# Kernel optimization log

Measured on AMD Instinct MI355X. Metric: run time of the kernel, lower is better.

Reference implementation:

```python
import jax, jax.numpy as jnp
import numpy as np
from math import tan, atan

N = 4_000_000
W_PX, H_PX = 1920, 1080
ZNEAR, ZFAR = 0.1, 100.0
FOVX = 1.0471975512  # 60 deg
FOVY = 2.0 * atan(tan(0.5 * FOVX) * H_PX / W_PX)
RELAX = 1.3


def _projection_matrix():
    # Camera.get_projection_matrix with left=-right, bottom=-top (offsets vanish)
    right = ZNEAR * tan(0.5 * FOVX)
    top = ZNEAR * tan(0.5 * FOVY)
    return np.array([
        [ZNEAR / right, 0.0, 0.0, 0.0],
        [0.0, ZNEAR / top, 0.0, 0.0],
        [0.0, 0.0, ZFAR / (ZFAR - ZNEAR), -ZFAR * ZNEAR / (ZFAR - ZNEAR)],
        [0.0, 0.0, 1.0, 0.0],
    ], dtype=np.float32)


def setup_inputs() -> dict:
    key = jax.random.key(0)
    k1, k2, k3 = jax.random.split(key, 3)
    # positions: xy spread in front of camera, z strictly positive (in-frustum-ish)
    xy = jax.random.uniform(k1, (N, 2), minval=-6.0, maxval=6.0, dtype=jnp.float32)
    z = jax.random.uniform(k2, (N, 1), minval=0.5, maxval=30.0, dtype=jnp.float32)
    pos3d = jnp.concatenate([xy, z], axis=1)  # (N,3)
    # symmetric PSD 3x3 covariances
    A = jax.random.normal(k3, (N, 3, 3), dtype=jnp.float32) * 0.1
    cov3d = A @ A.swapaxes(-1, -2)  # (N,3,3)
    view_matrix = jnp.eye(4, dtype=jnp.float32)  # world2model (camera at origin)
    projection_matrix = jnp.asarray(_projection_matrix())
    return {"pos3d": pos3d, "cov3d": cov3d,
            "view_matrix": view_matrix, "projection_matrix": projection_matrix}


def reference(pos3d, cov3d, view_matrix, projection_matrix):
    # --- project position with MVP (pos3d @ view.T then @ proj.T) ---
    Vt = view_matrix.T
    p_model = pos3d @ Vt[:3, :3] + Vt[3, :3]                       # (N,3)
    ones = jnp.ones((p_model.shape[0], 1), dtype=p_model.dtype)
    p_h = jnp.concatenate([p_model, ones], axis=1)                 # (N,4)
    p_clip = p_h @ projection_matrix.T                             # (N,4)
    p_ndc = p_clip[:, :3] / (p_clip[:, 3:4] + 1e-6)                # (N,3)

    # --- view-frustum cull mask ---
    mask = ((p_ndc[:, 2] >= 0.2)
            & (p_ndc[:, 0] >= -RELAX) & (p_ndc[:, 0] <= RELAX)
            & (p_ndc[:, 1] >= -RELAX) & (p_ndc[:, 1] <= RELAX))

    # --- screen-space position (masked; original gathers pos[mask], we keep full-N padded) ---
    sx = 0.5 * (p_ndc[:, 0] + 1.0) * W_PX
    sy = (1.0 - 0.5 * (p_ndc[:, 1] + 1.0)) * H_PX
    pos2d = jnp.where(mask[:, None], jnp.stack([sx, sy, p_ndc[:, 2]], axis=1), 0.0)

    # --- 2D covariance: J @ W @ cov3d @ W.T @ J.T ---
    Wm = view_matrix[:3, :3].T                                     # (3,3)
    x, y, z = pos3d[:, 0], pos3d[:, 1], pos3d[:, 2]
    inv_z = 1.0 / z
    zeros = jnp.zeros_like(z)
    J = jnp.stack([
        jnp.stack([inv_z, zeros, -x * inv_z], axis=1),
        jnp.stack([zeros, inv_z, -y * inv_z], axis=1),
    ], axis=1)                                                     # (N,2,3)
    M = jnp.einsum('ij,njk,lk->nil', Wm, cov3d, Wm)                # (N,3,3)
    cov2d = jnp.einsum('nij,njk,nlk->nil', J, M, J)                # (N,2,2)
    cov2d = jnp.where(mask[:, None, None], cov2d, 0.0)
    return pos2d, cov2d, mask
```

## Files before the change

### kernel.cpp

```cpp
#include <hip/hip_runtime.h>

#define PXW 1920.0f
#define PXH 1080.0f
#define RELAXF 1.3f

__global__ __launch_bounds__(256) void cam_kernel(
    const float* __restrict__ pos3d,
    const float* __restrict__ cov3d,
    const float* __restrict__ view,
    const float* __restrict__ proj,
    float* __restrict__ out,
    int n)
{
  const int g = blockIdx.x * blockDim.x + threadIdx.x;
  if (g * 4 >= n) return;

  float V[12];
  float P[16];
#pragma unroll
  for (int i = 0; i < 12; ++i) V[i] = view[i];
#pragma unroll
  for (int i = 0; i < 16; ++i) P[i] = proj[i];

  const float4* p4 = reinterpret_cast<const float4*>(pos3d) + (size_t)3 * g;
  const float4 pa = p4[0], pb = p4[1], pc = p4[2];
  float px[4], py[4], pz[4];
  px[0] = pa.x; py[0] = pa.y; pz[0] = pa.z;
  px[1] = pa.w; py[1] = pb.x; pz[1] = pb.y;
  px[2] = pb.z; py[2] = pb.w; pz[2] = pc.x;
  px[3] = pc.y; py[3] = pc.z; pz[3] = pc.w;

  const float4* c4 = reinterpret_cast<const float4*>(cov3d) + (size_t)9 * g;
  float cf[36];
#pragma unroll
  for (int i = 0; i < 9; ++i) {
    const float4 t = c4[i];
    cf[4 * i + 0] = t.x; cf[4 * i + 1] = t.y;
    cf[4 * i + 2] = t.z; cf[4 * i + 3] = t.w;
  }

  float o_pos[12];
  float o_cov[16];
  float o_msk[4];

#pragma unroll
  for (int k = 0; k < 4; ++k) {
    const float x = px[k], y = py[k], z = pz[k];

    const float pm0 = V[0] * x + V[1] * y + V[2]  * z + V[3];
    const float pm1 = V[4] * x + V[5] * y + V[6]  * z + V[7];
    const float pm2 = V[8] * x + V[9] * y + V[10] * z + V[11];

    const float c0 = P[0]  * pm0 + P[1]  * pm1 + P[2]  * pm2 + P[3];
    const float c1 = P[4]  * pm0 + P[5]  * pm1 + P[6]  * pm2 + P[7];
    const float c2 = P[8]  * pm0 + P[9]  * pm1 + P[10] * pm2 + P[11];
    const float c3 = P[12] * pm0 + P[13] * pm1 + P[14] * pm2 + P[15];

    const float iw = 1.0f / (c3 + 1e-6f);
    const float nx = c0 * iw, ny = c1 * iw, nz = c2 * iw;

    const bool m = (nz >= 0.2f) && (nx >= -RELAXF) && (nx <= RELAXF)
                                && (ny >= -RELAXF) && (ny <= RELAXF);

    const float sx = 0.5f * (nx + 1.0f) * PXW;
    const float sy = (1.0f - 0.5f * (ny + 1.0f)) * PXH;

    o_pos[3 * k + 0] = m ? sx : 0.0f;
    o_pos[3 * k + 1] = m ? sy : 0.0f;
    o_pos[3 * k + 2] = m ? nz : 0.0f;
    o_msk[k]         = m ? 1.0f : 0.0f;

    const float iz = 1.0f / z;
    const float a0 = iz * (V[0] - x * V[2]);
    const float a1 = iz * (V[4] - x * V[6]);
    const float a2 = iz * (V[8] - x * V[10]);
    const float b0 = iz * (V[1] - y * V[2]);
    const float b1 = iz * (V[5] - y * V[6]);
    const float b2 = iz * (V[9] - y * V[10]);

    const float* C = &cf[9 * k];
    const float u0 = C[0] * a0 + C[1] * a1 + C[2] * a2;
    const float u1 = C[3] * a0 + C[4] * a1 + C[5] * a2;
    const float u2 = C[6] * a0 + C[7] * a1 + C[8] * a2;
    const float v0 = C[0] * b0 + C[1] * b1 + C[2] * b2;
    const float v1 = C[3] * b0 + C[4] * b1 + C[5] * b2;
    const float v2 = C[6] * b0 + C[7] * b1 + C[8] * b2;

    const float c00 = a0 * u0 + a1 * u1 + a2 * u2;
    const float c01 = a0 * v0 + a1 * v1 + a2 * v2;
    const float c10 = b0 * u0 + b1 * u1 + b2 * u2;
    const float c11 = b0 * v0 + b1 * v1 + b2 * v2;

    o_cov[4 * k + 0] = m ? c00 : 0.0f;
    o_cov[4 * k + 1] = m ? c01 : 0.0f;
    o_cov[4 * k + 2] = m ? c10 : 0.0f;
    o_cov[4 * k + 3] = m ? c11 : 0.0f;
  }

  float4* op = reinterpret_cast<float4*>(out) + (size_t)3 * g;
  op[0] = make_float4(o_pos[0], o_pos[1], o_pos[2],  o_pos[3]);
  op[1] = make_float4(o_pos[4], o_pos[5], o_pos[6],  o_pos[7]);
  op[2] = make_float4(o_pos[8], o_pos[9], o_pos[10], o_pos[11]);

  float4* oc = reinterpret_cast<float4*>(out + (size_t)3 * n) + (size_t)4 * g;
#pragma unroll
  for (int k = 0; k < 4; ++k)
    oc[k] = make_float4(o_cov[4 * k + 0], o_cov[4 * k + 1],
                        o_cov[4 * k + 2], o_cov[4 * k + 3]);

  reinterpret_cast<float4*>(out + (size_t)7 * n)[g] =
      make_float4(o_msk[0], o_msk[1], o_msk[2], o_msk[3]);
}

extern "C" void kernel_launch(void* const* d_in, const int* in_sizes, int n_in,
                              void* d_out, int out_size, void* d_ws, size_t ws_size,
                              hipStream_t stream) {
  const float* pos3d = (const float*)d_in[0];
  const float* cov3d = (const float*)d_in[1];
  const float* view  = (const float*)d_in[2];
  const float* proj  = (const float*)d_in[3];

  const int n = in_sizes[0] / 3;

  const int ngroups = (n + 3) / 4;
  const int threads = 256;
  const int blocks  = (ngroups + threads - 1) / threads;

  cam_kernel<<<blocks, threads, 0, stream>>>(pos3d, cov3d, view, proj,
                                             (float*)d_out, n);
}
```

Before: 304.6 us.

## Stage pos/cov tiles through swizzled LDS for fully coalesced global loads and stores

Each block now handles a 1024-point tile. Threads load positions and covariances from global memory with lane-contiguous float4 accesses into shared memory, using an XOR swizzle to avoid bank conflicts, then read back their per-thread groups of four points. Outputs are staged through shared memory the same way so the global stores are coalesced, and a launch-bounds occupancy hint is added. This targets the strided per-thread float4 access pattern of the old kernel, at the cost of about 48KB of LDS per block, two extra barriers, and a duplicated tail path.

```diff
diff --git a/kernel.cpp b/kernel.cpp
--- a/kernel.cpp
+++ b/kernel.cpp
@@ -4,7 +4,16 @@
 #define PXH 1080.0f
 #define RELAXF 1.3f
 
-__global__ __launch_bounds__(256) void cam_kernel(
+#define NT 256
+#define TILE_PTS 1024
+#define POS_F4 768
+#define COV_F4 2304
+
+typedef float f4 __attribute__((ext_vector_type(4)));
+
+__device__ __forceinline__ int swz(int s) { return s ^ ((s >> 3) & 7); }
+
+__global__ __launch_bounds__(NT, 3) void cam_kernel(
     const float* __restrict__ pos3d,
     const float* __restrict__ cov3d,
     const float* __restrict__ view,
@@ -12,8 +21,12 @@
     float* __restrict__ out,
     int n)
 {
-  const int g = blockIdx.x * blockDim.x + threadIdx.x;
-  if (g * 4 >= n) return;
+  __shared__ f4 sPos[POS_F4];
+  __shared__ f4 sCov[COV_F4];
+
+  const int b = blockIdx.x;
+  const int t = threadIdx.x;
+  const long long p0 = (long long)b * TILE_PTS;
 
   float V[12];
   float P[16];
@@ -22,94 +35,188 @@
 #pragma unroll
   for (int i = 0; i < 16; ++i) P[i] = proj[i];
 
-  const float4* p4 = reinterpret_cast<const float4*>(pos3d) + (size_t)3 * g;
-  const float4 pa = p4[0], pb = p4[1], pc = p4[2];
-  float px[4], py[4], pz[4];
-  px[0] = pa.x; py[0] = pa.y; pz[0] = pa.z;
-  px[1] = pa.w; py[1] = pb.x; pz[1] = pb.y;
-  px[2] = pb.z; py[2] = pb.w; pz[2] = pc.x;
-  px[3] = pc.y; py[3] = pc.z; pz[3] = pc.w;
-
-  const float4* c4 = reinterpret_cast<const float4*>(cov3d) + (size_t)9 * g;
-  float cf[36];
-#pragma unroll
-  for (int i = 0; i < 9; ++i) {
-    const float4 t = c4[i];
-    cf[4 * i + 0] = t.x; cf[4 * i + 1] = t.y;
-    cf[4 * i + 2] = t.z; cf[4 * i + 3] = t.w;
+  if (p0 + TILE_PTS <= n) {
+    const f4* gp = reinterpret_cast<const f4*>(pos3d) + (size_t)POS_F4 * b;
+    const f4* gc = reinterpret_cast<const f4*>(cov3d) + (size_t)COV_F4 * b;
+    f4 rp[3], rc[9];
+#pragma unroll
+    for (int j = 0; j < 3; ++j) rp[j] = gp[t + NT * j];
+#pragma unroll
+    for (int j = 0; j < 9; ++j) rc[j] = gc[t + NT * j];
+#pragma unroll
+    for (int j = 0; j < 3; ++j) sPos[t + NT * j] = rp[j];
+#pragma unroll
+    for (int j = 0; j < 9; ++j) sCov[swz(t + NT * j)] = rc[j];
+    __syncthreads();
+
+    const f4 pa = sPos[3 * t + 0];
+    const f4 pb = sPos[3 * t + 1];
+    const f4 pc = sPos[3 * t + 2];
+    float cf[36];
+#pragma unroll
+    for (int j = 0; j < 9; ++j) {
+      const f4 c = sCov[swz(9 * t + j)];
+      cf[4 * j + 0] = c.x; cf[4 * j + 1] = c.y;
+      cf[4 * j + 2] = c.z; cf[4 * j + 3] = c.w;
+    }
+
+    float px[4], py[4], pz[4];
+    px[0] = pa.x; py[0] = pa.y; pz[0] = pa.z;
+    px[1] = pa.w; py[1] = pb.x; pz[1] = pb.y;
+    px[2] = pb.z; py[2] = pb.w; pz[2] = pc.x;
+    px[3] = pc.y; py[3] = pc.z; pz[3] = pc.w;
+
+    float o_pos[12], o_cov[16], o_msk[4];
+
+#pragma unroll
+    for (int k = 0; k < 4; ++k) {
+      const float x = px[k], y = py[k], z = pz[k];
+
+      const float pm0 = V[0] * x + V[1] * y + V[2]  * z + V[3];
+      const float pm1 = V[4] * x + V[5] * y + V[6]  * z + V[7];
+      const float pm2 = V[8] * x + V[9] * y + V[10] * z + V[11];
+
+      const float c0 = P[0]  * pm0 + P[1]  * pm1 + P[2]  * pm2 + P[3];
+      const float c1 = P[4]  * pm0 + P[5]  * pm1 + P[6]  * pm2 + P[7];
+      const float c2 = P[8]  * pm0 + P[9]  * pm1 + P[10] * pm2 + P[11];
+      const float c3 = P[12] * pm0 + P[13] * pm1 + P[14] * pm2 + P[15];
+
+      const float iw = 1.0f / (c3 + 1e-6f);
+      const float nx = c0 * iw, ny = c1 * iw, nz = c2 * iw;
+
+      const bool m = (nz >= 0.2f) && (nx >= -RELAXF) && (nx <= RELAXF)
+                                  && (ny >= -RELAXF) && (ny <= RELAXF);
+
+      const float sx = 0.5f * (nx + 1.0f) * PXW;
+      const float sy = (1.0f - 0.5f * (ny + 1.0f)) * PXH;
+
+      o_pos[3 * k + 0] = m ? sx : 0.0f;
+      o_pos[3 * k + 1] = m ? sy : 0.0f;
+      o_pos[3 * k + 2] = m ? nz : 0.0f;
+      o_msk[k]         = m ? 1.0f : 0.0f;
+
+      const float iz = 1.0f / z;
+      const float a0 = iz * (V[0] - x * V[2]);
+      const float a1 = iz * (V[4] - x * V[6]);
+      const float a2 = iz * (V[8] - x * V[10]);
+      const float b0 = iz * (V[1] - y * V[2]);
+      const float b1 = iz * (V[5] - y * V[6]);
+      const float b2 = iz * (V[9] - y * V[10]);
+
+      const float* C = &cf[9 * k];
+      const float u0 = C[0] * a0 + C[1] * a1 + C[2] * a2;
+      const float u1 = C[3] * a0 + C[4] * a1 + C[5] * a2;
+      const float u2 = C[6] * a0 + C[7] * a1 + C[8] * a2;
+      const float v0 = C[0] * b0 + C[1] * b1 + C[2] * b2;
+      const float v1 = C[3] * b0 + C[4] * b1 + C[5] * b2;
+      const float v2 = C[6] * b0 + C[7] * b1 + C[8] * b2;
+
+      o_cov[4 * k + 0] = m ? (a0 * u0 + a1 * u1 + a2 * u2) : 0.0f;
+      o_cov[4 * k + 1] = m ? (a0 * v0 + a1 * v1 + a2 * v2) : 0.0f;
+      o_cov[4 * k + 2] = m ? (b0 * u0 + b1 * u1 + b2 * u2) : 0.0f;
+      o_cov[4 * k + 3] = m ? (b0 * v0 + b1 * v1 + b2 * v2) : 0.0f;
+    }
+
+    f4 tm = { o_msk[0], o_msk[1], o_msk[2], o_msk[3] };
+    reinterpret_cast<f4*>(out + (size_t)7 * n)[(size_t)NT * b + t] = tm;
+
+    __syncthreads();
+#pragma unroll
+    for (int c = 0; c < 3; ++c) {
+      f4 v = { o_pos[4 * c + 0], o_pos[4 * c + 1],
+               o_pos[4 * c + 2], o_pos[4 * c + 3] };
+      sCov[swz(3 * t + c)] = v;
+    }
+#pragma unroll
+    for (int c = 0; c < 4; ++c) {
+      f4 v = { o_cov[4 * c + 0], o_cov[4 * c + 1],
+               o_cov[4 * c + 2], o_cov[4 * c + 3] };
+      sCov[swz(POS_F4 + 4 * t + c)] = v;
+    }
+    __syncthreads();
+
+    f4* opg = reinterpret_cast<f4*>(out) + (size_t)POS_F4 * b;
+#pragma unroll
+    for (int j = 0; j < 3; ++j) opg[t + NT * j] = sCov[swz(t + NT * j)];
+
+    f4* ocg = reinterpret_cast<f4*>(out + (size_t)3 * n) + (size_t)1024 * b;
+#pragma unroll
+    for (int j = 0; j < 4; ++j)
+      ocg[t + NT * j] = sCov[swz(POS_F4 + t + NT * j)];
+
+  } else {
+    for (long long g = p0 / 4 + t; 4 * g < n; g += NT) {
+      const float4* p4 = reinterpret_cast<const float4*>(pos3d) + (size_t)3 * g;
+      const float4 pa = p4[0], pb = p4[1], pc = p4[2];
+      float px[4], py[4], pz[4];
+      px[0] = pa.x; py[0] = pa.y; pz[0] = pa.z;
+      px[1] = pa.w; py[1] = pb.x; pz[1] = pb.y;
+      px[2] = pb.z; py[2] = pb.w; pz[2] = pc.x;
+      px[3] = pc.y; py[3] = pc.z; pz[3] = pc.w;
+
+      const float4* c4 = reinterpret_cast<const float4*>(cov3d) + (size_t)9 * g;
+      float cf[36];
+#pragma unroll
+      for (int i = 0; i < 9; ++i) {
+        const float4 tt = c4[i];
+        cf[4 * i + 0] = tt.x; cf[4 * i + 1] = tt.y;
+        cf[4 * i + 2] = tt.z; cf[4 * i + 3] = tt.w;
+      }
+
+      float o_pos[12], o_cov[16], o_msk[4];
+#pragma unroll
+      for (int k = 0; k < 4; ++k) {
+        const float x = px[k], y = py[k], z = pz[k];
+        const float pm0 = V[0] * x + V[1] * y + V[2]  * z + V[3];
+        const float pm1 = V[4] * x + V[5] * y + V[6]  * z + V[7];
+        const float pm2 = V[8] * x + V[9] * y + V[10] * z + V[11];
+        const float c0 = P[0]  * pm0 + P[1]  * pm1 + P[2]  * pm2 + P[3];
+        const float c1 = P[4]  * pm0 + P[5]  * pm1 + P[6]  * pm2 + P[7];
+        const float c2 = P[8]  * pm0 + P[9]  * pm1 + P[10] * pm2 + P[11];
+        const float c3 = P[12] * pm0 + P[13] * pm1 + P[14] * pm2 + P[15];
+        const float iw = 1.0f / (c3 + 1e-6f);
+        const float nx = c0 * iw, ny = c1 * iw, nz = c2 * iw;
+        const bool m = (nz >= 0.2f) && (nx >= -RELAXF) && (nx <= RELAXF)
+                                    && (ny >= -RELAXF) && (ny <= RELAXF);
+        const float sx = 0.5f * (nx + 1.0f) * PXW;
+        const float sy = (1.0f - 0.5f * (ny + 1.0f)) * PXH;
+        o_pos[3 * k + 0] = m ? sx : 0.0f;
+        o_pos[3 * k + 1] = m ? sy : 0.0f;
+        o_pos[3 * k + 2] = m ? nz : 0.0f;
+        o_msk[k]         = m ? 1.0f : 0.0f;
+        const float iz = 1.0f / z;
+        const float a0 = iz * (V[0] - x * V[2]);
+        const float a1 = iz * (V[4] - x * V[6]);
+        const float a2 = iz * (V[8] - x * V[10]);
+        const float b0 = iz * (V[1] - y * V[2]);
+        const float b1 = iz * (V[5] - y * V[6]);
+        const float b2 = iz * (V[9] - y * V[10]);
+        const float* C = &cf[9 * k];
+        const float u0 = C[0] * a0 + C[1] * a1 + C[2] * a2;
+        const float u1 = C[3] * a0 + C[4] * a1 + C[5] * a2;
+        const float u2 = C[6] * a0 + C[7] * a1 + C[8] * a2;
+        const float v0 = C[0] * b0 + C[1] * b1 + C[2] * b2;
+        const float v1 = C[3] * b0 + C[4] * b1 + C[5] * b2;
+        const float v2 = C[6] * b0 + C[7] * b1 + C[8] * b2;
+        o_cov[4 * k + 0] = m ? (a0 * u0 + a1 * u1 + a2 * u2) : 0.0f;
+        o_cov[4 * k + 1] = m ? (a0 * v0 + a1 * v1 + a2 * v2) : 0.0f;
+        o_cov[4 * k + 2] = m ? (b0 * u0 + b1 * u1 + b2 * u2) : 0.0f;
+        o_cov[4 * k + 3] = m ? (b0 * v0 + b1 * v1 + b2 * v2) : 0.0f;
+      }
+
+      float4* op = reinterpret_cast<float4*>(out) + (size_t)3 * g;
+      op[0] = make_float4(o_pos[0], o_pos[1], o_pos[2],  o_pos[3]);
+      op[1] = make_float4(o_pos[4], o_pos[5], o_pos[6],  o_pos[7]);
+      op[2] = make_float4(o_pos[8], o_pos[9], o_pos[10], o_pos[11]);
+      float4* oc = reinterpret_cast<float4*>(out + (size_t)3 * n) + (size_t)4 * g;
+#pragma unroll
+      for (int k = 0; k < 4; ++k)
+        oc[k] = make_float4(o_cov[4 * k + 0], o_cov[4 * k + 1],
+                            o_cov[4 * k + 2], o_cov[4 * k + 3]);
+      reinterpret_cast<float4*>(out + (size_t)7 * n)[g] =
+          make_float4(o_msk[0], o_msk[1], o_msk[2], o_msk[3]);
+    }
   }
-
-  float o_pos[12];
-  float o_cov[16];
-  float o_msk[4];
-
-#pragma unroll
-  for (int k = 0; k < 4; ++k) {
-    const float x = px[k], y = py[k], z = pz[k];
-
-    const float pm0 = V[0] * x + V[1] * y + V[2]  * z + V[3];
-    const float pm1 = V[4] * x + V[5] * y + V[6]  * z + V[7];
-    const float pm2 = V[8] * x + V[9] * y + V[10] * z + V[11];
-
-    const float c0 = P[0]  * pm0 + P[1]  * pm1 + P[2]  * pm2 + P[3];
-    const float c1 = P[4]  * pm0 + P[5]  * pm1 + P[6]  * pm2 + P[7];
-    const float c2 = P[8]  * pm0 + P[9]  * pm1 + P[10] * pm2 + P[11];
-    const float c3 = P[12] * pm0 + P[13] * pm1 + P[14] * pm2 + P[15];
-
-    const float iw = 1.0f / (c3 + 1e-6f);
-    const float nx = c0 * iw, ny = c1 * iw, nz = c2 * iw;
-
-    const bool m = (nz >= 0.2f) && (nx >= -RELAXF) && (nx <= RELAXF)
-                                && (ny >= -RELAXF) && (ny <= RELAXF);
-
-    const float sx = 0.5f * (nx + 1.0f) * PXW;
-    const float sy = (1.0f - 0.5f * (ny + 1.0f)) * PXH;
-
-    o_pos[3 * k + 0] = m ? sx : 0.0f;
-    o_pos[3 * k + 1] = m ? sy : 0.0f;
-    o_pos[3 * k + 2] = m ? nz : 0.0f;
-    o_msk[k]         = m ? 1.0f : 0.0f;
-
-    const float iz = 1.0f / z;
-    const float a0 = iz * (V[0] - x * V[2]);
-    const float a1 = iz * (V[4] - x * V[6]);
-    const float a2 = iz * (V[8] - x * V[10]);
-    const float b0 = iz * (V[1] - y * V[2]);
-    const float b1 = iz * (V[5] - y * V[6]);
-    const float b2 = iz * (V[9] - y * V[10]);
-
-    const float* C = &cf[9 * k];
-    const float u0 = C[0] * a0 + C[1] * a1 + C[2] * a2;
-    const float u1 = C[3] * a0 + C[4] * a1 + C[5] * a2;
-    const float u2 = C[6] * a0 + C[7] * a1 + C[8] * a2;
-    const float v0 = C[0] * b0 + C[1] * b1 + C[2] * b2;
-    const float v1 = C[3] * b0 + C[4] * b1 + C[5] * b2;
-    const float v2 = C[6] * b0 + C[7] * b1 + C[8] * b2;
-
-    const float c00 = a0 * u0 + a1 * u1 + a2 * u2;
-    const float c01 = a0 * v0 + a1 * v1 + a2 * v2;
-    const float c10 = b0 * u0 + b1 * u1 + b2 * u2;
-    const float c11 = b0 * v0 + b1 * v1 + b2 * v2;
-
-    o_cov[4 * k + 0] = m ? c00 : 0.0f;
-    o_cov[4 * k + 1] = m ? c01 : 0.0f;
-    o_cov[4 * k + 2] = m ? c10 : 0.0f;
-    o_cov[4 * k + 3] = m ? c11 : 0.0f;
-  }
-
-  float4* op = reinterpret_cast<float4*>(out) + (size_t)3 * g;
-  op[0] = make_float4(o_pos[0], o_pos[1], o_pos[2],  o_pos[3]);
-  op[1] = make_float4(o_pos[4], o_pos[5], o_pos[6],  o_pos[7]);
-  op[2] = make_float4(o_pos[8], o_pos[9], o_pos[10], o_pos[11]);
-
-  float4* oc = reinterpret_cast<float4*>(out + (size_t)3 * n) + (size_t)4 * g;
-#pragma unroll
-  for (int k = 0; k < 4; ++k)
-    oc[k] = make_float4(o_cov[4 * k + 0], o_cov[4 * k + 1],
-                        o_cov[4 * k + 2], o_cov[4 * k + 3]);
-
-  reinterpret_cast<float4*>(out + (size_t)7 * n)[g] =
-      make_float4(o_msk[0], o_msk[1], o_msk[2], o_msk[3]);
 }
 
 extern "C" void kernel_launch(void* const* d_in, const int* in_sizes, int n_in,
@@ -122,10 +229,7 @@
 
   const int n = in_sizes[0] / 3;
 
-  const int ngroups = (n + 3) / 4;
-  const int threads = 256;
-  const int blocks  = (ngroups + threads - 1) / threads;
-
-  cam_kernel<<<blocks, threads, 0, stream>>>(pos3d, cov3d, view, proj,
-                                             (float*)d_out, n);
+  const int blocks = (n + TILE_PTS - 1) / TILE_PTS;
+  cam_kernel<<<blocks, NT, 0, stream>>>(pos3d, cov3d, view, proj,
+                                        (float*)d_out, n);
 }
```

Result: faster. 278.8 us (-8.5%).
